# Kernel optimization log

Measured on AMD Instinct MI355X. Metric: run time of the kernel, lower is better.

## Reference

```python
import jax, jax.numpy as jnp
import numpy as np

D = 1024
H = 16
HD = D // H  # 64


def setup_inputs() -> dict:
    key = jax.random.key(0)
    ks = jax.random.split(key, 11)
    B, L = 2, 2048
    std = 0.02
    return {
        "query": jax.random.normal(ks[0], (B, L, D), jnp.float32),
        "key": jax.random.normal(ks[1], (B, L, D), jnp.float32),
        "value": jax.random.normal(ks[2], (B, L, D), jnp.float32),
        "Wq": jax.random.normal(ks[3], (D, D), jnp.float32) * std,
        "bq": jnp.zeros((D,), jnp.float32),
        "Wk": jax.random.normal(ks[4], (D, D), jnp.float32) * std,
        "bk": jnp.zeros((D,), jnp.float32),
        "Wv": jax.random.normal(ks[5], (D, D), jnp.float32) * std,
        "bv": jnp.zeros((D,), jnp.float32),
        "Wo": jax.random.normal(ks[6], (D, D), jnp.float32) * std,
        "bo": jnp.zeros((D,), jnp.float32),
    }


def _split_heads(x):
    # [B, L, D] -> [B, H, L, HD]
    B, L, _ = x.shape
    return x.reshape(B, L, H, HD).transpose(0, 2, 1, 3)


def reference(query, key, value, Wq, bq, Wk, bk, Wv, bv, Wo, bo):
    B, Lq, _ = query.shape
    # Linear projections (torch Linear: x @ W.T + b)
    Q = _split_heads(query @ Wq.T + bq)
    K = _split_heads(key @ Wk.T + bk)
    V = _split_heads(value @ Wv.T + bv)
    scale = HD ** -0.5
    scores = jnp.einsum("bhqd,bhkd->bhqk", Q, K) * scale  # [B,H,Lq,Lk]
    weights = jax.nn.softmax(scores, axis=-1)
    attended = jnp.einsum("bhqk,bhkd->bhqd", weights, V)  # [B,H,Lq,HD]
    attended = attended.transpose(0, 2, 1, 3).reshape(B, Lq, D)
    output = attended @ Wo.T + bo
    return output, weights.mean(axis=1)
```

## Files before the change

kernel.cpp:

```cpp
#include <hip/hip_runtime.h>
#include <stdint.h>

#define D_MODEL 1024
#define NHEAD 16
#define HDIM 64
#define SEQ 2048
#define NTOK 4096
#define KVB 128
#define NT (KVB / 16)

typedef unsigned short u16;
typedef float f32x4 __attribute__((ext_vector_type(4)));
typedef __bf16 bf16x8 __attribute__((ext_vector_type(8)));
typedef unsigned int u32x4 __attribute__((ext_vector_type(4)));
typedef u16 u16x4 __attribute__((ext_vector_type(4)));

#define QSC 0.180336880111117f

__device__ __forceinline__ u16 fcast_bf(float f) {
  __bf16 h = (__bf16)f;
  return __builtin_bit_cast(u16, h);
}

__device__ __forceinline__ float exp2_fast(float x) {
#if __has_builtin(__builtin_amdgcn_exp2f)
  return __builtin_amdgcn_exp2f(x);
#else
  return __expf(x * 0.69314718056f);
#endif
}

__device__ __forceinline__ bf16x8 scale_q(bf16x8 q) {
  bf16x8 r;
#pragma unroll
  for (int i = 0; i < 8; i++) r[i] = (__bf16)((float)q[i] * QSC);
  return r;
}

__device__ __forceinline__ bf16x8 lds_frag(const u16* sm, int off) {
  return *reinterpret_cast<const bf16x8*>(sm + off);
}

__device__ __forceinline__ void gload_lds16(const u16* g, u16* l) {
  __builtin_amdgcn_global_load_lds((const __attribute__((address_space(1))) void*)g,
                                   (__attribute__((address_space(3))) void*)l, 16, 0, 0);
}

__global__ void cvt_all_kernel(const float* __restrict__ q, const float* __restrict__ k,
                               const float* __restrict__ v, const float* __restrict__ wq,
                               const float* __restrict__ wk, const float* __restrict__ wv,
                               const float* __restrict__ wo, u16* __restrict__ dst) {
  const int y = blockIdx.y;
  const float* s = y == 0 ? q : (y == 1 ? k : (y == 2 ? v : (y == 3 ? wq :
                   (y == 4 ? wk : (y == 5 ? wv : wo)))));
  const int n4 = y < 3 ? 1048576 : 262144;
  const size_t off4 = y < 3 ? (size_t)y * 1048576 : 3145728 + (size_t)(y - 3) * 262144;
  u16x4* d = reinterpret_cast<u16x4*>(dst) + off4;
  int i = blockIdx.x * blockDim.x + threadIdx.x;
  int stride = gridDim.x * blockDim.x;
  for (; i < n4; i += stride) {
    f32x4 vv = reinterpret_cast<const f32x4*>(s)[i];
    u16x4 o;
    o[0] = fcast_bf(vv[0]); o[1] = fcast_bf(vv[1]);
    o[2] = fcast_bf(vv[2]); o[3] = fcast_bf(vv[3]);
    d[i] = o;
  }
}

__global__ __launch_bounds__(256)
void gemm_qkv_kernel(const u16* __restrict__ Abase, const u16* __restrict__ Wbase,
                     const float* __restrict__ b0, const float* __restrict__ b1,
                     const float* __restrict__ b2, u16* __restrict__ obf) {
  const int z = blockIdx.z;
  const u16* A = Abase + (size_t)z * NTOK * D_MODEL;
  const u16* W = Wbase + (size_t)z * D_MODEL * D_MODEL;
  const float* bias = z == 0 ? b0 : (z == 1 ? b1 : b2);
  u16* oz = obf + (size_t)z * NTOK * D_MODEL;

  const int flat = blockIdx.y * 8 + blockIdx.x;
  const int nf = (flat & 7) * 32 + (flat >> 3);
  const int bn0 = (nf & 7) * 128;
  const int bm0 = (nf >> 3) * 128;
  const int tid = threadIdx.x;
  const int lane = tid & 63, wid = tid >> 6;
  const int wm = wid >> 1, wn = wid & 1;
  const int l15 = lane & 15, l4 = lane >> 4;
  const int lrow8 = lane >> 3, lch = lane & 7;

  __shared__ u16 smA[128 * 64];
  __shared__ u16 smB[128 * 64];

  f32x4 acc[4][4];
#pragma unroll
  for (int mi = 0; mi < 4; mi++)
#pragma unroll
    for (int ni = 0; ni < 4; ni++) acc[mi][ni] = f32x4{0.f, 0.f, 0.f, 0.f};

  for (int it = 0; it < D_MODEL / 64; it++) {
    const int k0 = it * 64;
    __syncthreads();
#pragma unroll
    for (int c2 = 0; c2 < 4; c2++) {
      int blk = wid * 4 + c2;
      int base16 = blk * 512;
      int row = blk * 8 + lrow8;
      gload_lds16(A + (size_t)(bm0 + row) * D_MODEL + k0 + lch * 8, &smA[base16]);
      gload_lds16(W + (size_t)(bn0 + row) * D_MODEL + k0 + lch * 8, &smB[base16]);
    }
    __syncthreads();
#pragma unroll
    for (int kk = 0; kk < 2; kk++) {
      bf16x8 af[4], bfv[4];
#pragma unroll
      for (int mi = 0; mi < 4; mi++) {
        int r = wm * 64 + mi * 16 + l15;
        af[mi] = lds_frag(smA, r * 64 + (kk * 4 + l4) * 8);
      }
#pragma unroll
      for (int ni = 0; ni < 4; ni++) {
        int r = wn * 64 + ni * 16 + l15;
        bfv[ni] = lds_frag(smB, r * 64 + (kk * 4 + l4) * 8);
      }
#pragma unroll
      for (int mi = 0; mi < 4; mi++)
#pragma unroll
        for (int ni = 0; ni < 4; ni++)
          acc[mi][ni] = __builtin_amdgcn_mfma_f32_16x16x32_bf16(af[mi], bfv[ni], acc[mi][ni], 0, 0, 0);
    }
  }

#pragma unroll
  for (int mi = 0; mi < 4; mi++) {
#pragma unroll
    for (int ni = 0; ni < 4; ni++) {
      int colg = bn0 + wn * 64 + ni * 16 + l15;
      float bv = bias[colg];
      if (z == 2) {
        int h = colg >> 6, hd = colg & 63;
        int row0 = bm0 + wm * 64 + mi * 16 + l4 * 4;
        int b = row0 >> 11, lq = row0 & 2047;
        u16x4 pk;
#pragma unroll
        for (int j = 0; j < 4; j++) pk[j] = fcast_bf(acc[mi][ni][j] + bv);
        size_t idx = ((size_t)((b * NHEAD + h) * HDIM + hd)) * SEQ + lq;
        *reinterpret_cast<u16x4*>(oz + idx) = pk;
      } else {
#pragma unroll
        for (int j = 0; j < 4; j++) {
          int rowg = bm0 + wm * 64 + mi * 16 + l4 * 4 + j;
          float v = acc[mi][ni][j] + bv;
          int b = rowg >> 11, lq = rowg & 2047;
          int h = colg >> 6, hd = colg & 63;
          oz[((size_t)((b * NHEAD + h) * SEQ + lq)) * HDIM + hd] = fcast_bf(v);
        }
      }
    }
  }
}

__global__ __launch_bounds__(512)
void attn_kernel(const u16* __restrict__ Qh, const u16* __restrict__ Kh,
                 const u16* __restrict__ Vh, u16* __restrict__ attb,
                 float* __restrict__ m_ws, float* __restrict__ linv_ws) {
  const int qt0 = blockIdx.x * 128;
  const int bh = blockIdx.y;
  const int b = bh >> 4, h = bh & 15;
  const int tid = threadIdx.x;
  const int lane = tid & 63, wid = tid >> 6;
  const int l15 = lane & 15, l4 = lane >> 4;

  const u16* Qp = Qh + (size_t)bh * SEQ * HDIM;
  const u16* Kp = Kh + (size_t)bh * SEQ * HDIM;
  const u16* Vp = Vh + (size_t)bh * HDIM * SEQ;

  __shared__ u16 smK[KVB * 64];
  __shared__ u16 smV[64 * KVB];
  __shared__ u16 smP[8][16 * KVB];

  bf16x8 qf[2];
  {
    const u16* qrow = Qp + (size_t)(qt0 + wid * 16 + l15) * HDIM;
    qf[0] = scale_q(*reinterpret_cast<const bf16x8*>(qrow + l4 * 8));
    qf[1] = scale_q(*reinterpret_cast<const bf16x8*>(qrow + 32 + l4 * 8));
  }

  float m = -1e30f, lsum = 0.f;
  f32x4 oacc[4];
#pragma unroll
  for (int d = 0; d < 4; d++) oacc[d] = f32x4{0.f, 0.f, 0.f, 0.f};

  u32x4 rk[2], rv[2];
#pragma unroll
  for (int i = 0; i < 2; i++) {
    int c = i * 512 + tid;
    rk[i] = *reinterpret_cast<const u32x4*>(Kp + (size_t)(c >> 3) * HDIM + (c & 7) * 8);
    rv[i] = *reinterpret_cast<const u32x4*>(Vp + (size_t)(c >> 4) * SEQ + (c & 15) * 8);
  }

  for (int kt = 0; kt < SEQ / KVB; kt++) {
    __syncthreads();
#pragma unroll
    for (int i = 0; i < 2; i++) {
      int c = i * 512 + tid;
      { int row = c >> 3, ch = c & 7;
        *reinterpret_cast<u32x4*>(&smK[row * 64 + ((ch ^ (row & 7)) * 8)]) = rk[i]; }
      { int row = c >> 4, ch = c & 15;
        *reinterpret_cast<u32x4*>(&smV[row * KVB + ((ch ^ (row & 15)) * 8)]) = rv[i]; }
    }
    __syncthreads();
    if (kt + 1 < SEQ / KVB) {
      int kn = (kt + 1) * KVB;
#pragma unroll
      for (int i = 0; i < 2; i++) {
        int c = i * 512 + tid;
        rk[i] = *reinterpret_cast<const u32x4*>(Kp + (size_t)(kn + (c >> 3)) * HDIM + (c & 7) * 8);
        rv[i] = *reinterpret_cast<const u32x4*>(Vp + (size_t)(c >> 4) * SEQ + kn + (c & 15) * 8);
      }
    }
    f32x4 s[NT];
#pragma unroll
    for (int nt = 0; nt < NT; nt++) s[nt] = f32x4{0.f, 0.f, 0.f, 0.f};
#pragma unroll
    for (int kk = 0; kk < 2; kk++) {
#pragma unroll
      for (int nt = 0; nt < NT; nt++) {
        int r = nt * 16 + l15;
        int ch = (kk * 4 + l4) ^ (r & 7);
        bf16x8 kf = lds_frag(smK, r * 64 + ch * 8);
        s[nt] = __builtin_amdgcn_mfma_f32_16x16x32_bf16(kf, qf[kk], s[nt], 0, 0, 0);
      }
    }
    float smax = s[0][0];
#pragma unroll
    for (int nt = 0; nt < NT; nt++)
#pragma unroll
      for (int j = 0; j < 4; j++) smax = fmaxf(smax, s[nt][j]);
    smax = fmaxf(smax, __shfl_xor(smax, 16));
    smax = fmaxf(smax, __shfl_xor(smax, 32));
    float mn = fmaxf(m, smax);
    float corr = exp2_fast(m - mn);
    m = mn;
    float ps = 0.f;
#pragma unroll
    for (int nt = 0; nt < NT; nt++) {
      u16x4 pwv;
#pragma unroll
      for (int j = 0; j < 4; j++) {
        float pv = exp2_fast(s[nt][j] - mn);
        ps += pv;
        pwv[j] = fcast_bf(pv);
      }
      int sp = (nt * 4 + l4) ^ (l15 * 2);
      *reinterpret_cast<u16x4*>(&smP[wid][l15 * KVB + sp * 4]) = pwv;
    }
    ps += __shfl_xor(ps, 16);
    ps += __shfl_xor(ps, 32);
    lsum = lsum * corr + ps;
#pragma unroll
    for (int d = 0; d < 4; d++)
#pragma unroll
      for (int j = 0; j < 4; j++) oacc[d][j] *= corr;
#pragma unroll
    for (int kc = 0; kc < 4; kc++) {
      int chp = (kc * 4 + l4) ^ l15;
      bf16x8 pf = lds_frag(smP[wid], l15 * KVB + chp * 8);
#pragma unroll
      for (int d = 0; d < 4; d++) {
        int r = d * 16 + l15;
        int ch = (kc * 4 + l4) ^ (r & 15);
        bf16x8 vf = lds_frag(smV, r * KVB + ch * 8);
        oacc[d] = __builtin_amdgcn_mfma_f32_16x16x32_bf16(vf, pf, oacc[d], 0, 0, 0);
      }
    }
  }

  const float li = 1.f / lsum;
  const int token = qt0 + wid * 16 + l15;
  if (l4 == 0) {
    m_ws[(size_t)bh * SEQ + token] = m;
    linv_ws[(size_t)bh * SEQ + token] = li;
  }
#pragma unroll
  for (int d = 0; d < 4; d++) {
    u16x4 pk;
#pragma unroll
    for (int j = 0; j < 4; j++) pk[j] = fcast_bf(oacc[d][j] * li);
    *reinterpret_cast<u16x4*>(
        attb + ((size_t)(b * SEQ + token)) * D_MODEL + h * HDIM + d * 16 + l4 * 4) = pk;
  }
}

__global__ __launch_bounds__(512)
void tail_kernel(const u16* __restrict__ Qh, const u16* __restrict__ Kh,
                 const float* __restrict__ m_ws, const float* __restrict__ linv_ws,
                 float* __restrict__ out1,
                 const u16* __restrict__ attb, const u16* __restrict__ Wo,
                 const float* __restrict__ bo, float* __restrict__ out0) {
  __shared__ u16 smem[16384];
  const int bid = blockIdx.x;
  const int tid = threadIdx.x;
  const int lane = tid & 63, wid = tid >> 6;
  const int l15 = lane & 15, l4 = lane >> 4;

  if (bid < 512) {
    const int kt0 = (bid & 15) * 128;
    const int qt0 = ((bid >> 4) & 15) * 128;
    const int b = bid >> 8;

    f32x4 macc[2][4];
#pragma unroll
    for (int t = 0; t < 2; t++)
#pragma unroll
      for (int nt = 0; nt < 4; nt++) macc[t][nt] = f32x4{0.f, 0.f, 0.f, 0.f};

    const int rbase = qt0 + wid * 16 + l4 * 4;
    const size_t qoff = (size_t)(qt0 + wid * 16 + l15) * HDIM;
    const int srow = tid >> 3, sch = tid & 7;
    const int soff = srow * 64 + ((sch ^ (srow & 7)) * 8);

    u32x4 rk[2];
    bf16x8 qfa, qfb;
    {
      const u16* Kp0 = Kh + (size_t)(b * NHEAD) * SEQ * HDIM;
#pragma unroll
      for (int t = 0; t < 2; t++)
        rk[t] = *reinterpret_cast<const u32x4*>(Kp0 + (size_t)(kt0 + t * 64 + srow) * HDIM + sch * 8);
      const u16* Qp0 = Qh + (size_t)(b * NHEAD) * SEQ * HDIM + qoff;
      qfa = scale_q(*reinterpret_cast<const bf16x8*>(Qp0 + l4 * 8));
      qfb = scale_q(*reinterpret_cast<const bf16x8*>(Qp0 + 32 + l4 * 8));
    }

    for (int h = 0; h < NHEAD; h++) {
      const int bh = b * NHEAD + h;
#pragma unroll
      for (int t = 0; t < 2; t++)
        *reinterpret_cast<u32x4*>(&smem[((h & 1) * 2 + t) * 4096 + soff]) = rk[t];
      __syncthreads();
      u32x4 rkn[2];
      bf16x8 qfan, qfbn;
      if (h + 1 < NHEAD) {
        const u16* Kp1 = Kh + (size_t)(bh + 1) * SEQ * HDIM;
#pragma unroll
        for (int t = 0; t < 2; t++)
          rkn[t] = *reinterpret_cast<const u32x4*>(Kp1 + (size_t)(kt0 + t * 64 + srow) * HDIM + sch * 8);
        const u16* Qp1 = Qh + (size_t)(bh + 1) * SEQ * HDIM + qoff;
        qfan = scale_q(*reinterpret_cast<const bf16x8*>(Qp1 + l4 * 8));
        qfbn = scale_q(*reinterpret_cast<const bf16x8*>(Qp1 + 32 + l4 * 8));
      }
      f32x4 mv = *reinterpret_cast<const f32x4*>(&m_ws[(size_t)bh * SEQ + rbase]);
      f32x4 lv = *reinterpret_cast<const f32x4*>(&linv_ws[(size_t)bh * SEQ + rbase]);
#pragma unroll
      for (int t = 0; t < 2; t++) {
        const u16* kbuf = &smem[((h & 1) * 2 + t) * 4096];
        f32x4 s[4];
#pragma unroll
        for (int nt = 0; nt < 4; nt++) s[nt] = f32x4{0.f, 0.f, 0.f, 0.f};
#pragma unroll
        for (int kk = 0; kk < 2; kk++) {
#pragma unroll
          for (int nt = 0; nt < 4; nt++) {
            int r = nt * 16 + l15;
            int ch = (kk * 4 + l4) ^ (r & 7);
            bf16x8 kf = lds_frag(kbuf, r * 64 + ch * 8);
            s[nt] = __builtin_amdgcn_mfma_f32_16x16x32_bf16(kk == 0 ? qfa : qfb, kf, s[nt], 0, 0, 0);
          }
        }
#pragma unroll
        for (int nt = 0; nt < 4; nt++)
#pragma unroll
          for (int j = 0; j < 4; j++)
            macc[t][nt][j] += exp2_fast(s[nt][j] - mv[j]) * lv[j];
      }
      if (h + 1 < NHEAD) {
        rk[0] = rkn[0]; rk[1] = rkn[1];
        qfa = qfan; qfb = qfbn;
      }
    }
    const float invh = 1.f / 16.f;
#pragma unroll
    for (int t = 0; t < 2; t++)
#pragma unroll
      for (int nt = 0; nt < 4; nt++)
#pragma unroll
        for (int j = 0; j < 4; j++)
          out1[((size_t)(b * SEQ + rbase + j)) * SEQ + kt0 + t * 64 + nt * 16 + l15] =
              macc[t][nt][j] * invh;
  } else {
    const int flat = bid - 512;
    const int nf = (flat & 7) * 32 + (flat >> 3);
    const int bn0 = (nf & 7) * 128;
    const int bm0 = (nf >> 3) * 128;
    const int wm = wid >> 1, wn = wid & 1;
    const int lrow8 = lane >> 3, lch = lane & 7;
    u16* smA = smem;
    u16* smB = smem + 8192;

    f32x4 acc[2][4];
#pragma unroll
    for (int mi = 0; mi < 2; mi++)
#pragma unroll
      for (int ni = 0; ni < 4; ni++) acc[mi][ni] = f32x4{0.f, 0.f, 0.f, 0.f};

    for (int it = 0; it < D_MODEL / 64; it++) {
      const int k0 = it * 64;
      __syncthreads();
#pragma unroll
      for (int c2 = 0; c2 < 2; c2++) {
        int blk = wid * 2 + c2;
        int base16 = blk * 512;
        int row = blk * 8 + lrow8;
        gload_lds16(attb + (size_t)(bm0 + row) * D_MODEL + k0 + lch * 8, &smA[base16]);
        gload_lds16(Wo + (size_t)(bn0 + row) * D_MODEL + k0 + lch * 8, &smB[base16]);
      }
      __syncthreads();
#pragma unroll
      for (int kk = 0; kk < 2; kk++) {
        bf16x8 af[2], bfv[4];
#pragma unroll
        for (int mi = 0; mi < 2; mi++) {
          int r = wm * 32 + mi * 16 + l15;
          af[mi] = lds_frag(smA, r * 64 + (kk * 4 + l4) * 8);
        }
#pragma unroll
        for (int ni = 0; ni < 4; ni++) {
          int r = wn * 64 + ni * 16 + l15;
          bfv[ni] = lds_frag(smB, r * 64 + (kk * 4 + l4) * 8);
        }
#pragma unroll
        for (int mi = 0; mi < 2; mi++)
#pragma unroll
          for (int ni = 0; ni < 4; ni++)
            acc[mi][ni] = __builtin_amdgcn_mfma_f32_16x16x32_bf16(af[mi], bfv[ni], acc[mi][ni], 0, 0, 0);
      }
    }

#pragma unroll
    for (int mi = 0; mi < 2; mi++) {
#pragma unroll
      for (int ni = 0; ni < 4; ni++) {
        int colg = bn0 + wn * 64 + ni * 16 + l15;
        float bv = bo[colg];
#pragma unroll
        for (int j = 0; j < 4; j++) {
          int rowg = bm0 + wm * 32 + mi * 16 + l4 * 4 + j;
          out0[(size_t)rowg * D_MODEL + colg] = acc[mi][ni][j] + bv;
        }
      }
    }
  }
}

extern "C" void kernel_launch(void* const* d_in, const int* in_sizes, int n_in,
                              void* d_out, int out_size, void* d_ws, size_t ws_size,
                              hipStream_t stream) {
  (void)in_sizes; (void)n_in; (void)out_size; (void)ws_size;
  const float* query = (const float*)d_in[0];
  const float* key = (const float*)d_in[1];
  const float* value = (const float*)d_in[2];
  const float* Wq = (const float*)d_in[3];
  const float* bq = (const float*)d_in[4];
  const float* Wk = (const float*)d_in[5];
  const float* bk = (const float*)d_in[6];
  const float* Wv = (const float*)d_in[7];
  const float* bv = (const float*)d_in[8];
  const float* Wo = (const float*)d_in[9];
  const float* bo = (const float*)d_in[10];

  char* ws = (char*)d_ws;
  u16* xb = (u16*)(ws);
  u16* wb = (u16*)(ws + 25165824);
  u16* Qhp = (u16*)(ws + 33554432);
  u16* attb = (u16*)(ws + 58720256);
  float* m_ws = (float*)(ws + 67108864);
  float* linv_ws = (float*)(ws + 67371008);

  float* out0 = (float*)d_out;
  float* out1 = out0 + (size_t)NTOK * D_MODEL;

  cvt_all_kernel<<<dim3(256, 7), 256, 0, stream>>>(query, key, value, Wq, Wk, Wv, Wo, xb);

  gemm_qkv_kernel<<<dim3(8, 32, 3), 256, 0, stream>>>(xb, wb, bq, bk, bv, Qhp);
  attn_kernel<<<dim3(16, 32), 512, 0, stream>>>(Qhp, Qhp + 4194304, Qhp + 8388608,
                                                attb, m_ws, linv_ws);
  tail_kernel<<<768, 512, 0, stream>>>(Qhp, Qhp + 4194304, m_ws, linv_ws, out1,
                                       attb, wb + 3 * 1048576, bo, out0);
}
```

Measured before the change: 185.8 us.

## Split weights-mean tiles in half and load K fragments directly from global

The head-averaged attention-weights branch of the tail kernel now uses 128x64 tiles instead of 128x128, doubling its block count from 512 to 1024. It also drops the LDS staging, double buffering and per-head __syncthreads, and instead has each wave load its K MFMA fragments straight from global memory. The goal is more parallelism and no barrier stalls in the recompute-softmax-and-average pass. The cost is that every wave redundantly loads the same K tile, and the head loop is no longer software-prefetched, so global latency is exposed on each head.

```diff
diff --git a/kernel.cpp b/kernel.cpp
--- a/kernel.cpp
+++ b/kernel.cpp
@@ -302,91 +302,57 @@
   const int lane = tid & 63, wid = tid >> 6;
   const int l15 = lane & 15, l4 = lane >> 4;
 
-  if (bid < 512) {
-    const int kt0 = (bid & 15) * 128;
-    const int qt0 = ((bid >> 4) & 15) * 128;
-    const int b = bid >> 8;
-
-    f32x4 macc[2][4];
-#pragma unroll
-    for (int t = 0; t < 2; t++)
-#pragma unroll
-      for (int nt = 0; nt < 4; nt++) macc[t][nt] = f32x4{0.f, 0.f, 0.f, 0.f};
+  if (bid < 1024) {
+    const int kt0 = (bid & 31) * 64;
+    const int qt0 = ((bid >> 5) & 15) * 128;
+    const int b = bid >> 9;
 
     const int rbase = qt0 + wid * 16 + l4 * 4;
-    const size_t qoff = (size_t)(qt0 + wid * 16 + l15) * HDIM;
-    const int srow = tid >> 3, sch = tid & 7;
-    const int soff = srow * 64 + ((sch ^ (srow & 7)) * 8);
-
-    u32x4 rk[2];
-    bf16x8 qfa, qfb;
-    {
-      const u16* Kp0 = Kh + (size_t)(b * NHEAD) * SEQ * HDIM;
-#pragma unroll
-      for (int t = 0; t < 2; t++)
-        rk[t] = *reinterpret_cast<const u32x4*>(Kp0 + (size_t)(kt0 + t * 64 + srow) * HDIM + sch * 8);
-      const u16* Qp0 = Qh + (size_t)(b * NHEAD) * SEQ * HDIM + qoff;
-      qfa = scale_q(*reinterpret_cast<const bf16x8*>(Qp0 + l4 * 8));
-      qfb = scale_q(*reinterpret_cast<const bf16x8*>(Qp0 + 32 + l4 * 8));
-    }
-
+    const size_t hstride = (size_t)SEQ * HDIM;
+    const u16* Kp = Kh + (size_t)(b * NHEAD) * hstride + (size_t)(kt0 + l15) * HDIM + l4 * 8;
+    const u16* Qp = Qh + (size_t)(b * NHEAD) * hstride +
+                    (size_t)(qt0 + wid * 16 + l15) * HDIM + l4 * 8;
+    const float* mp = m_ws + (size_t)(b * NHEAD) * SEQ + rbase;
+    const float* lp = linv_ws + (size_t)(b * NHEAD) * SEQ + rbase;
+
+    f32x4 macc[4];
+#pragma unroll
+    for (int nt = 0; nt < 4; nt++) macc[nt] = f32x4{0.f, 0.f, 0.f, 0.f};
+
+#pragma unroll 1
     for (int h = 0; h < NHEAD; h++) {
-      const int bh = b * NHEAD + h;
-#pragma unroll
-      for (int t = 0; t < 2; t++)
-        *reinterpret_cast<u32x4*>(&smem[((h & 1) * 2 + t) * 4096 + soff]) = rk[t];
-      __syncthreads();
-      u32x4 rkn[2];
-      bf16x8 qfan, qfbn;
-      if (h + 1 < NHEAD) {
-        const u16* Kp1 = Kh + (size_t)(bh + 1) * SEQ * HDIM;
-#pragma unroll
-        for (int t = 0; t < 2; t++)
-          rkn[t] = *reinterpret_cast<const u32x4*>(Kp1 + (size_t)(kt0 + t * 64 + srow) * HDIM + sch * 8);
-        const u16* Qp1 = Qh + (size_t)(bh + 1) * SEQ * HDIM + qoff;
-        qfan = scale_q(*reinterpret_cast<const bf16x8*>(Qp1 + l4 * 8));
-        qfbn = scale_q(*reinterpret_cast<const bf16x8*>(Qp1 + 32 + l4 * 8));
-      }
-      f32x4 mv = *reinterpret_cast<const f32x4*>(&m_ws[(size_t)bh * SEQ + rbase]);
-      f32x4 lv = *reinterpret_cast<const f32x4*>(&linv_ws[(size_t)bh * SEQ + rbase]);
-#pragma unroll
-      for (int t = 0; t < 2; t++) {
-        const u16* kbuf = &smem[((h & 1) * 2 + t) * 4096];
-        f32x4 s[4];
-#pragma unroll
-        for (int nt = 0; nt < 4; nt++) s[nt] = f32x4{0.f, 0.f, 0.f, 0.f};
-#pragma unroll
-        for (int kk = 0; kk < 2; kk++) {
-#pragma unroll
-          for (int nt = 0; nt < 4; nt++) {
-            int r = nt * 16 + l15;
-            int ch = (kk * 4 + l4) ^ (r & 7);
-            bf16x8 kf = lds_frag(kbuf, r * 64 + ch * 8);
-            s[nt] = __builtin_amdgcn_mfma_f32_16x16x32_bf16(kk == 0 ? qfa : qfb, kf, s[nt], 0, 0, 0);
-          }
-        }
+      const u16* Kn = Kp + (size_t)h * hstride;
+      const u16* Qn = Qp + (size_t)h * hstride;
+      bf16x8 kf[8];
+#pragma unroll
+      for (int f = 0; f < 8; f++)
+        kf[f] = *reinterpret_cast<const bf16x8*>(Kn + (size_t)(f & 3) * 16 * HDIM + (f >> 2) * 32);
+      bf16x8 qa = scale_q(*reinterpret_cast<const bf16x8*>(Qn));
+      bf16x8 qb = scale_q(*reinterpret_cast<const bf16x8*>(Qn + 32));
+      f32x4 mv = *reinterpret_cast<const f32x4*>(mp + (size_t)h * SEQ);
+      f32x4 lv = *reinterpret_cast<const f32x4*>(lp + (size_t)h * SEQ);
+      f32x4 s[4];
+#pragma unroll
+      for (int nt = 0; nt < 4; nt++) s[nt] = f32x4{0.f, 0.f, 0.f, 0.f};
+#pragma unroll
+      for (int kk = 0; kk < 2; kk++)
 #pragma unroll
         for (int nt = 0; nt < 4; nt++)
-#pragma unroll
-          for (int j = 0; j < 4; j++)
-            macc[t][nt][j] += exp2_fast(s[nt][j] - mv[j]) * lv[j];
-      }
-      if (h + 1 < NHEAD) {
-        rk[0] = rkn[0]; rk[1] = rkn[1];
-        qfa = qfan; qfb = qfbn;
-      }
+          s[nt] = __builtin_amdgcn_mfma_f32_16x16x32_bf16(kk ? qb : qa, kf[kk * 4 + nt], s[nt], 0, 0, 0);
+#pragma unroll
+      for (int nt = 0; nt < 4; nt++)
+#pragma unroll
+        for (int j = 0; j < 4; j++)
+          macc[nt][j] += exp2_fast(s[nt][j] - mv[j]) * lv[j];
     }
     const float invh = 1.f / 16.f;
 #pragma unroll
-    for (int t = 0; t < 2; t++)
-#pragma unroll
-      for (int nt = 0; nt < 4; nt++)
-#pragma unroll
-        for (int j = 0; j < 4; j++)
-          out1[((size_t)(b * SEQ + rbase + j)) * SEQ + kt0 + t * 64 + nt * 16 + l15] =
-              macc[t][nt][j] * invh;
+    for (int nt = 0; nt < 4; nt++)
+#pragma unroll
+      for (int j = 0; j < 4; j++)
+        out1[((size_t)(b * SEQ + rbase + j)) * SEQ + kt0 + nt * 16 + l15] = macc[nt][j] * invh;
   } else {
-    const int flat = bid - 512;
+    const int flat = bid - 1024;
     const int nf = (flat & 7) * 32 + (flat >> 3);
     const int bn0 = (nf & 7) * 128;
     const int bm0 = (nf >> 3) * 128;
@@ -482,6 +448,6 @@
   gemm_qkv_kernel<<<dim3(8, 32, 3), 256, 0, stream>>>(xb, wb, bq, bk, bv, Qhp);
   attn_kernel<<<dim3(16, 32), 512, 0, stream>>>(Qhp, Qhp + 4194304, Qhp + 8388608,
                                                 attb, m_ws, linv_ws);
-  tail_kernel<<<768, 512, 0, stream>>>(Qhp, Qhp + 4194304, m_ws, linv_ws, out1,
-                                       attb, wb + 3 * 1048576, bo, out0);
-}
+  tail_kernel<<<1280, 512, 0, stream>>>(Qhp, Qhp + 4194304, m_ws, linv_ws, out1,
+                                        attb, wb + 3 * 1048576, bo, out0);
+}
```

Result: slower. 279.4 us (+50.3%).
